# Performance work log

Measured on AMD Instinct MI355X. Metric: run time of the kernel, lower is better.

Reference implementation:

```python
import jax, jax.numpy as jnp
import numpy as np

H = W = 28          # image side, from reshape([28, 28]) in the original
Q = 32768           # parameter dimension of the linear filtration p
CARD = 50           # max persistence pairs
D = 2               # image rank


def setup_inputs() -> dict:
    key = jax.random.key(0)
    k1, k2, k3, k4, k5 = jax.random.split(key, 5)
    X = jax.random.normal(k1, (H * W, Q), dtype=jnp.float32)
    Y = jax.random.normal(k2, (H * W, Q), dtype=jnp.float32)
    p = jax.random.normal(k3, (Q,), dtype=jnp.float32)
    # Indices of (birth, death) top-dimensional cells produced by the gudhi
    # CubicalComplex numpy_function. They are ints wrapped in stop_gradient in
    # the original graph, i.e. constants w.r.t. the differentiable math, so we
    # model them as random in-range coordinates: 2*D*CARD flat entries, each an
    # index in [0, 28).
    inds1 = jax.random.randint(k4, (2 * D * CARD,), 0, H, dtype=jnp.int32)
    inds2 = jax.random.randint(k5, (2 * D * CARD,), 0, H, dtype=jnp.int32)
    return {"X": X, "Y": Y, "p": p, "inds1": inds1, "inds2": inds2}


def _gather_dgm(img, inds):
    # gather_nd(img, reshape(inds, [-1, 2])) then reshape to [-1, 2]
    ij = inds.reshape(-1, D)                 # [2*CARD, 2]
    vals = img[ij[:, 0], ij[:, 1]]           # [2*CARD]
    return vals.reshape(-1, 2)               # [CARD, 2] (birth, death) pairs


def reference(X, Y, p, inds1, inds2):
    Xp = (X @ p).reshape(H, W)               # tensordot(X, p, 1) -> [28, 28]
    Yp = (Y @ p).reshape(H, W)
    dgm1 = _gather_dgm(Xp, inds1)
    dgm2 = _gather_dgm(Yp, inds2)
    return dgm1, dgm2
```

## Files before the change

kernel.cpp:

```cpp
#include <hip/hip_runtime.h>
#include <hip/hip_bf16.h>


#define QDIM   32768
#define SPLIT  8
#define CHUNK4 (QDIM / SPLIT / 4)

__global__ __launch_bounds__(256) void dot_gather(
        const float* __restrict__ X,
        const float* __restrict__ Y,
        const float* __restrict__ p,
        const int* __restrict__ inds1,
        const int* __restrict__ inds2,
        float* __restrict__ out) {
    const int b = blockIdx.x;
    const int k = b >> 3;
    const int c = b & 7;

    int i, j;
    const float* M;
    if (k < 100) {
        i = inds1[2 * k];
        j = inds1[2 * k + 1];
        M = X;
    } else {
        const int kk = k - 100;
        i = inds2[2 * kk];
        j = inds2[2 * kk + 1];
        M = Y;
    }
    const int row = i * 28 + j;

    const float4* __restrict__ a4 =
        (const float4*)(M + (size_t)row * QDIM) + (size_t)c * CHUNK4;
    const float4* __restrict__ p4 =
        (const float4*)p + (size_t)c * CHUNK4;

    const int t = threadIdx.x;
    float4 a0 = a4[t];
    float4 b0 = p4[t];
    float4 a1 = a4[t + 256];
    float4 b1 = p4[t + 256];
    float4 a2 = a4[t + 512];
    float4 b2 = p4[t + 512];
    float4 a3 = a4[t + 768];
    float4 b3 = p4[t + 768];

    float s0 = a0.x * b0.x + a0.y * b0.y + a0.z * b0.z + a0.w * b0.w;
    float s1 = a1.x * b1.x + a1.y * b1.y + a1.z * b1.z + a1.w * b1.w;
    float s2 = a2.x * b2.x + a2.y * b2.y + a2.z * b2.z + a2.w * b2.w;
    float s3 = a3.x * b3.x + a3.y * b3.y + a3.z * b3.z + a3.w * b3.w;
    float sum = (s0 + s1) + (s2 + s3);

    for (int off = 32; off > 0; off >>= 1)
        sum += __shfl_down(sum, off, 64);

    __shared__ float smem[4];
    const int lane = t & 63;
    const int wid  = t >> 6;
    if (lane == 0) smem[wid] = sum;
    __syncthreads();
    if (t == 0) {
        float blk = (smem[0] + smem[1]) + (smem[2] + smem[3]);
        atomicAdd(out + k, blk);
    }
}

extern "C" void kernel_launch(void* const* d_in, const int* in_sizes, int n_in,
                              void* d_out, int out_size, void* d_ws, size_t ws_size,
                              hipStream_t stream) {
    const float* X     = (const float*)d_in[0];
    const float* Y     = (const float*)d_in[1];
    const float* p     = (const float*)d_in[2];
    const int*   inds1 = (const int*)d_in[3];
    const int*   inds2 = (const int*)d_in[4];
    float* out = (float*)d_out;

    hipMemsetAsync(out, 0, 200 * sizeof(float), stream);
    dot_gather<<<200 * SPLIT, 256, 0, stream>>>(X, Y, p, inds1, inds2, out);
}
```

Baseline: 180.1 us.

## Use one block per gathered dot product, drop memset and atomics

Each gathered output now gets one 256-thread block that loops over the full 32768-length row, instead of eight blocks each covering a chunk and combining with atomicAdd. This removes the hipMemsetAsync launch and the atomic accumulation, and the result is written directly. The cost is a much smaller grid (200 blocks instead of 1600), so there is less memory-level parallelism for what is a bandwidth-bound read of about 26 MB and fewer waves in flight per CU.

```diff
diff --git a/kernel.cpp b/kernel.cpp
--- a/kernel.cpp
+++ b/kernel.cpp
@@ -3,8 +3,8 @@
 
 
 #define QDIM   32768
-#define SPLIT  8
-#define CHUNK4 (QDIM / SPLIT / 4)
+#define Q4     (QDIM / 4)
+#define NPTS   100
 
 __global__ __launch_bounds__(256) void dot_gather(
         const float* __restrict__ X,
@@ -13,43 +13,42 @@
         const int* __restrict__ inds1,
         const int* __restrict__ inds2,
         float* __restrict__ out) {
-    const int b = blockIdx.x;
-    const int k = b >> 3;
-    const int c = b & 7;
+    const int k = blockIdx.x;
 
     int i, j;
     const float* M;
-    if (k < 100) {
+    if (k < NPTS) {
         i = inds1[2 * k];
         j = inds1[2 * k + 1];
         M = X;
     } else {
-        const int kk = k - 100;
+        const int kk = k - NPTS;
         i = inds2[2 * kk];
         j = inds2[2 * kk + 1];
         M = Y;
     }
     const int row = i * 28 + j;
 
-    const float4* __restrict__ a4 =
-        (const float4*)(M + (size_t)row * QDIM) + (size_t)c * CHUNK4;
-    const float4* __restrict__ p4 =
-        (const float4*)p + (size_t)c * CHUNK4;
+    const float4* __restrict__ a4 = (const float4*)(M + (size_t)row * QDIM);
+    const float4* __restrict__ p4 = (const float4*)p;
 
     const int t = threadIdx.x;
-    float4 a0 = a4[t];
-    float4 b0 = p4[t];
-    float4 a1 = a4[t + 256];
-    float4 b1 = p4[t + 256];
-    float4 a2 = a4[t + 512];
-    float4 b2 = p4[t + 512];
-    float4 a3 = a4[t + 768];
-    float4 b3 = p4[t + 768];
-
-    float s0 = a0.x * b0.x + a0.y * b0.y + a0.z * b0.z + a0.w * b0.w;
-    float s1 = a1.x * b1.x + a1.y * b1.y + a1.z * b1.z + a1.w * b1.w;
-    float s2 = a2.x * b2.x + a2.y * b2.y + a2.z * b2.z + a2.w * b2.w;
-    float s3 = a3.x * b3.x + a3.y * b3.y + a3.z * b3.z + a3.w * b3.w;
+    float s0 = 0.f, s1 = 0.f, s2 = 0.f, s3 = 0.f;
+#pragma unroll 8
+    for (int i4 = 0; i4 < Q4 / 256; i4 += 4) {
+        float4 a0 = a4[t + (i4 + 0) * 256];
+        float4 b0 = p4[t + (i4 + 0) * 256];
+        float4 a1 = a4[t + (i4 + 1) * 256];
+        float4 b1 = p4[t + (i4 + 1) * 256];
+        float4 a2 = a4[t + (i4 + 2) * 256];
+        float4 b2 = p4[t + (i4 + 2) * 256];
+        float4 a3 = a4[t + (i4 + 3) * 256];
+        float4 b3 = p4[t + (i4 + 3) * 256];
+        s0 += a0.x * b0.x + a0.y * b0.y + a0.z * b0.z + a0.w * b0.w;
+        s1 += a1.x * b1.x + a1.y * b1.y + a1.z * b1.z + a1.w * b1.w;
+        s2 += a2.x * b2.x + a2.y * b2.y + a2.z * b2.z + a2.w * b2.w;
+        s3 += a3.x * b3.x + a3.y * b3.y + a3.z * b3.z + a3.w * b3.w;
+    }
     float sum = (s0 + s1) + (s2 + s3);
 
     for (int off = 32; off > 0; off >>= 1)
@@ -60,10 +59,8 @@
     const int wid  = t >> 6;
     if (lane == 0) smem[wid] = sum;
     __syncthreads();
-    if (t == 0) {
-        float blk = (smem[0] + smem[1]) + (smem[2] + smem[3]);
-        atomicAdd(out + k, blk);
-    }
+    if (t == 0)
+        out[k] = (smem[0] + smem[1]) + (smem[2] + smem[3]);
 }
 
 extern "C" void kernel_launch(void* const* d_in, const int* in_sizes, int n_in,
@@ -76,6 +73,5 @@
     const int*   inds2 = (const int*)d_in[4];
     float* out = (float*)d_out;
 
-    hipMemsetAsync(out, 0, 200 * sizeof(float), stream);
-    dot_gather<<<200 * SPLIT, 256, 0, stream>>>(X, Y, p, inds1, inds2, out);
+    dot_gather<<<2 * NPTS, 256, 0, stream>>>(X, Y, p, inds1, inds2, out);
 }
```

After: 179.3 us. Within noise of the previous version (-0.4%).
